# Performance work log

Measured on AMD Instinct MI355X. Metric: run time of the kernel, lower is better.

The kernel has to match this reference:

```python
import jax, jax.numpy as jnp
import numpy as np

NUM_HEADS = 16
DIM = 1024
HID = DIM // NUM_HEADS
B, S = 2, 2048
NEG_INF = -1e30


def setup_inputs() -> dict:
    key = jax.random.key(0)
    ks = jax.random.split(key, 8)
    def xavier(k, shape, fan_in, fan_out):
        limit = np.sqrt(6.0 / (fan_in + fan_out))
        return jax.random.uniform(k, shape, jnp.float32, -limit, limit)
    return {
        "q": jax.random.normal(ks[0], (B, S, DIM), jnp.float32),
        "k": jax.random.normal(ks[1], (B, S, DIM), jnp.float32),
        "v": jax.random.normal(ks[2], (B, S, DIM), jnp.float32),
        "Wq": xavier(ks[3], (1, NUM_HEADS, DIM, HID), DIM, HID),
        "Wk": xavier(ks[4], (1, NUM_HEADS, DIM, HID), DIM, HID),
        "Wv": xavier(ks[5], (1, NUM_HEADS, DIM, HID), DIM, HID),
        "Wo": xavier(ks[6], (1, DIM, DIM), DIM, DIM),
        "mask": jax.random.randint(ks[7], (B, S), 0, 2, jnp.int32),
    }


def reference(q, k, v, Wq, Wk, Wv, Wo, mask):
    b, s, d = q.shape
    norm = jnp.sqrt(jnp.asarray(HID, q.dtype))
    # per-head projections: [B,S,D] x [H,D,hd] -> [B,H,S,hd]
    qh = jnp.einsum('bsd,hde->bhse', q, Wq[0])
    kh = jnp.einsum('bsd,hde->bhse', k, Wk[0])
    vh = jnp.einsum('bsd,hde->bhse', v, Wv[0])
    scores = jnp.einsum('bhse,bhte->bhst', qh, kh) / norm  # [B,H,S,S]
    m = mask.astype(bool)
    # original fills masked rows AND cols with 0.0 (not -inf)
    pad = m[:, None, :, None] | m[:, None, None, :]
    scores = jnp.where(pad, 0.0, scores)
    causal = jnp.triu(jnp.ones((s, s), bool), 1)
    scores = jnp.where(causal, NEG_INF, scores)
    attn = jax.nn.softmax(scores, axis=-1)
    out = jnp.einsum('bhst,bhte->bhse', attn, vh)  # [B,H,S,hd]
    # faithful to original: raw view (memory reinterpretation), NO head transpose
    out = out.reshape(b, s, NUM_HEADS * HID)
    return out @ Wo[0]
```

## Files before the change

kernel.cpp:

```cpp
#include <hip/hip_runtime.h>
#include <hip/hip_bf16.h>

#define BB 2
#define SS 2048
#define DD 1024
#define HH 16
#define HD 64

typedef __attribute__((ext_vector_type(8))) short bf16x8;
typedef __attribute__((ext_vector_type(4))) float floatx4;

__device__ __forceinline__ short f2bf(float x) {
  __hip_bfloat16 h = __float2bfloat16(x);
  return __builtin_bit_cast(short, h);
}

__device__ __forceinline__ unsigned cvtpk_bf16(float lo, float hi) {
  unsigned r;
  asm("v_cvt_pk_bf16_f32 %0, %1, %2" : "=v"(r) : "v"(lo), "v"(hi));
  return r;
}

__device__ __forceinline__ void load_lds16(const void* g, void* l) {
  __builtin_amdgcn_global_load_lds(
      (const __attribute__((address_space(1))) unsigned int*)g,
      (__attribute__((address_space(3))) unsigned int*)l, 16, 0, 0);
}

__device__ __forceinline__ float redsum16(float v) {
  v += __shfl_xor(v, 1, 64);
  v += __shfl_xor(v, 2, 64);
  v += __shfl_xor(v, 4, 64);
  v += __shfl_xor(v, 8, 64);
  return v;
}

__global__ __launch_bounds__(256) void prep(
    const float* __restrict__ q, const float* __restrict__ k,
    const float* __restrict__ v, const float* __restrict__ Wq,
    const float* __restrict__ Wk, const float* __restrict__ Wv,
    const float* __restrict__ Wo, short* __restrict__ qo,
    short* __restrict__ ko, short* __restrict__ vo, short* __restrict__ qT,
    short* __restrict__ kT, short* __restrict__ vT, short* __restrict__ WoT) {
  __shared__ short sT[64 * 72];
  const int blk = blockIdx.x;
  if (blk < 12288) {
    const int which = blk >> 12, x = blk & 4095;
    const float* src = which == 0 ? q : which == 1 ? k : v;
    short* dst       = which == 0 ? qo : which == 1 ? ko : vo;
    size_t i = ((size_t)x * 256 + threadIdx.x) * 4;
    float4 f = *(const float4*)(src + i);
    short4 s;
    s.x = f2bf(f.x); s.y = f2bf(f.y); s.z = f2bf(f.z); s.w = f2bf(f.w);
    *(short4*)(dst + i) = s;
    return;
  }
  const int t = threadIdx.x, r = t >> 2, c0 = (t & 3) * 16;
  const float* src;
  short* dst;
  if (blk < 13056) {
    const int b2 = blk - 12288, which = b2 >> 8, rr = b2 & 255;
    const int dtile = rr & 15, h = rr >> 4, d0 = dtile * 64;
    const float* W = which == 0 ? Wq : which == 1 ? Wk : Wv;
    short* WT      = which == 0 ? qT : which == 1 ? kT : vT;
    src = W + ((size_t)h * DD + d0 + r) * HD + c0;
    dst = WT + ((size_t)h * HD + r) * DD + d0 + c0;
  } else {
    const int b3 = blk - 13056;
    const int k0 = (b3 & 15) * 64, n0 = (b3 >> 4) * 64;
    src = Wo + (size_t)(k0 + r) * DD + n0 + c0;
    dst = WoT + (size_t)(n0 + r) * DD + k0 + c0;
  }
  const float4* s4 = (const float4*)src;
  float4 f0 = s4[0], f1 = s4[1], f2 = s4[2], f3 = s4[3];
  const float ff[16] = {f0.x, f0.y, f0.z, f0.w, f1.x, f1.y, f1.z, f1.w,
                        f2.x, f2.y, f2.z, f2.w, f3.x, f3.y, f3.z, f3.w};
#pragma unroll
  for (int j = 0; j < 16; ++j) sT[r * 72 + c0 + j] = f2bf(ff[j]);
  __syncthreads();
  alignas(16) short tmp[16];
#pragma unroll
  for (int j = 0; j < 16; ++j) tmp[j] = sT[(c0 + j) * 72 + r];
  *(int4*)(dst) = *(const int4*)(tmp);
  *(int4*)(dst + 8) = *(const int4*)(tmp + 8);
}

__global__ __launch_bounds__(256) void proj(
    const short* __restrict__ xq, const short* __restrict__ xk,
    const short* __restrict__ xv, const short* __restrict__ WqT,
    const short* __restrict__ WkT, const short* __restrict__ WvT,
    const int* __restrict__ mask, short* __restrict__ qh,
    short* __restrict__ kh, short* __restrict__ vhT) {
  __shared__ union {
    struct {
      short A[2][128 * 32];
      short B[2][128 * 32];
    } s;
    short tr[64 * 136];
  } u;
  const int xcd = blockIdx.x & 7, tt = blockIdx.x >> 3;
  const int which = tt >> 5;
  const int rest = tt & 31;
  const int j = ((xcd & 3) << 1) | (rest >> 4);
  const int i = ((xcd >> 2) << 4) | (rest & 15);
  const short* X  = which == 0 ? xq : which == 1 ? xk : xv;
  const short* WT = which == 0 ? WqT : which == 1 ? WkT : WvT;
  const int m0 = i * 128, n0 = j * 128;
  const int tid = threadIdx.x, wid = tid >> 6, lane = tid & 63;
  const int quad = lane >> 4, l16 = lane & 15;
  const int wr = wid >> 1, wc = wid & 1;

  auto stage = [&](int buf, int k0) {
#pragma unroll
    for (int ii = 0; ii < 2; ++ii) {
      const int c = wid * 2 + ii;
      const int ci = c * 64 + lane;
      load_lds16(X + (size_t)(m0 + (ci >> 2)) * DD + k0 + (ci & 3) * 8,
                 &u.s.A[buf][c * 512]);
      load_lds16(WT + (size_t)(n0 + (ci >> 2)) * DD + k0 + (ci & 3) * 8,
                 &u.s.B[buf][c * 512]);
    }
  };

  floatx4 acc[4][4] = {};
  stage(0, 0);
  __syncthreads();
  int cur = 0;
  for (int k0 = 0; k0 < DD; k0 += 32) {
    if (k0 + 32 < DD) stage(cur ^ 1, k0 + 32);
    bf16x8 af[4], bfr[4];
#pragma unroll
    for (int mi = 0; mi < 4; ++mi)
      af[mi] =
          *(const bf16x8*)&u.s.A[cur][(wr * 64 + mi * 16 + l16) * 32 +
                                      quad * 8];
#pragma unroll
    for (int ni = 0; ni < 4; ++ni)
      bfr[ni] =
          *(const bf16x8*)&u.s.B[cur][(wc * 64 + ni * 16 + l16) * 32 +
                                      quad * 8];
#pragma unroll
    for (int mi = 0; mi < 4; ++mi)
#pragma unroll
      for (int ni = 0; ni < 4; ++ni)
        acc[mi][ni] = __builtin_amdgcn_mfma_f32_16x16x32_bf16(
            af[mi], bfr[ni], acc[mi][ni], 0, 0, 0);
    __syncthreads();
    cur ^= 1;
  }

  if (which != 2) {
    short* dst = which == 0 ? qh : kh;
    const float scale = (which == 0) ? 0.18033688f : 1.0f;
#pragma unroll
    for (int mi = 0; mi < 4; ++mi)
#pragma unroll
      for (int r2 = 0; r2 < 4; ++r2) {
        const int m = m0 + wr * 64 + mi * 16 + quad * 4 + r2;
        const float rs = mask[m] ? 0.f : scale;
#pragma unroll
        for (int ni = 0; ni < 4; ++ni) {
          const int n = n0 + wc * 64 + ni * 16 + l16;
          dst[(size_t)m * DD + n] = f2bf(acc[mi][ni][r2] * rs);
        }
      }
  } else {
    const int b = m0 >> 11;
#pragma unroll
    for (int p = 0; p < 2; ++p) {
      if (wc == p) {
#pragma unroll
        for (int mi = 0; mi < 4; ++mi)
#pragma unroll
          for (int ni = 0; ni < 4; ++ni)
#pragma unroll
            for (int r2 = 0; r2 < 4; ++r2) {
              const int ml = wr * 64 + mi * 16 + quad * 4 + r2;
              const int nl = ni * 16 + l16;
              u.tr[nl * 136 + ml] = f2bf(acc[mi][ni][r2]);
            }
      }
      __syncthreads();
      const int row = tid >> 2, part = tid & 3;
      const int gn = n0 + p * 64 + row;
      const int h = gn >> 6, e = gn & 63;
      short* dstp = vhT + ((size_t)(b * HH + h) * HD + e) * SS + (m0 & 2047) +
                    part * 32;
      const short* srcl = &u.tr[row * 136 + part * 32];
#pragma unroll
      for (int jj = 0; jj < 4; ++jj)
        *(int4*)(dstp + jj * 8) = *(const int4*)(srcl + jj * 8);
      if (p == 0) __syncthreads();
    }
  }
}

__global__ __launch_bounds__(256, 2) void attn(
    const short* __restrict__ qh, const short* __restrict__ kh,
    const short* __restrict__ vhT, short* __restrict__ X) {
  __shared__ short sm[16384 + 4 * 1152];
  const int tid = threadIdx.x, wid = tid >> 6, lane = tid & 63;
  const int quad = lane >> 4, l16 = lane & 15;
  const int xcd = blockIdx.x & 7, slot = blockIdx.x >> 3;
  const int bh = (xcd << 2) | (slot & 3);
  const int iblk = 31 - (slot >> 2);
  const int nt = iblk + 1;
  const int b = bh >> 4, h = bh & 15;
  const int r0 = iblk * 64;
  const int wrow = r0 + wid * 16;

  const short* Q  = qh + (size_t)b * SS * DD + h * HD;
  const short* K  = kh + (size_t)b * SS * DD + h * HD;
  const short* Vt = vhT + (size_t)bh * HD * SS;
  short* sPw = &sm[16384 + wid * 1152];
  const int swz = (l16 & 7) << 3;

  const int sr0 = tid >> 3, ss0 = (tid & 7) ^ (sr0 & 7);
  const int sr1 = (tid + 256) >> 3, ss1 = (tid & 7) ^ (sr1 & 7);
  const short* pK0 = K + (size_t)sr0 * DD + ss0 * 8;
  const short* pK1 = K + (size_t)sr1 * DD + ss1 * 8;
  const short* pV0 = Vt + (size_t)sr0 * SS + ss0 * 8;
  const short* pV1 = Vt + (size_t)sr1 * SS + ss1 * 8;

  auto stage = [&](int buf, int t) {
    const size_t ko = (size_t)t * 64 * DD;
    const int tc = t * 64;
    short* base = &sm[buf * 8192];
    load_lds16(pK0 + ko, base + tid * 8);
    load_lds16(pK1 + ko, base + 2048 + tid * 8);
    load_lds16(pV0 + tc, base + 4096 + tid * 8);
    load_lds16(pV1 + tc, base + 6144 + tid * 8);
  };

  bf16x8 aq[2];
#pragma unroll
  for (int ks = 0; ks < 2; ++ks)
    aq[ks] = *(const bf16x8*)(Q + (size_t)(wrow + l16) * DD + ks * 32 +
                              quad * 8);

  floatx4 o[4] = {};
  float lacc[4] = {};

  stage(0, 0);
  __syncthreads();
  int cur = 0;
  for (int t = 0; t < nt; ++t) {
    if (t + 1 < nt) stage(cur ^ 1, t + 1);
    const short* kb = &sm[cur * 8192];
    const short* vb = kb + 4096;
    bf16x8 bk[4][2];
#pragma unroll
    for (int ni = 0; ni < 4; ++ni)
#pragma unroll
      for (int ks = 0; ks < 2; ++ks)
        bk[ni][ks] = *(const bf16x8*)&kb[(ni * 16 + l16) * 64 +
                                         ((ks * 32 + quad * 8) ^ swz)];
    floatx4 s[4] = {};
#pragma unroll
    for (int ks = 0; ks < 2; ++ks)
#pragma unroll
      for (int ni = 0; ni < 4; ++ni)
        s[ni] = __builtin_amdgcn_mfma_f32_16x16x32_bf16(aq[ks], bk[ni][ks],
                                                        s[ni], 0, 0, 0);
    const bool diag = (t == nt - 1);
    const int t0 = t * 64;
#pragma unroll
    for (int ni = 0; ni < 4; ++ni)
#pragma unroll
      for (int r2p = 0; r2p < 2; ++r2p) {
        float p0 = __builtin_amdgcn_exp2f(s[ni][2 * r2p]);
        float p1 = __builtin_amdgcn_exp2f(s[ni][2 * r2p + 1]);
        if (diag) {
          const int row = wrow + quad * 4 + 2 * r2p;
          const int col = t0 + ni * 16 + l16;
          if (col > row) p0 = 0.f;
          if (col > row + 1) p1 = 0.f;
        }
        lacc[2 * r2p] += p0;
        lacc[2 * r2p + 1] += p1;
        const unsigned pk = cvtpk_bf16(p0, p1);
        short* wp = &sPw[(quad * 4 + 2 * r2p) * 72 + ni * 16 + l16];
        wp[0] = (short)pk;
        wp[72] = (short)(pk >> 16);
      }
#pragma unroll
    for (int ks = 0; ks < 2; ++ks) {
      const bf16x8 ap =
          *(const bf16x8*)&sPw[l16 * 72 + ks * 32 + quad * 8];
#pragma unroll
      for (int ei = 0; ei < 4; ++ei) {
        const bf16x8 bv = *(const bf16x8*)&vb[(ei * 16 + l16) * 64 +
                                              ((ks * 32 + quad * 8) ^ swz)];
        o[ei] = __builtin_amdgcn_mfma_f32_16x16x32_bf16(ap, bv, o[ei], 0, 0,
                                                        0);
      }
    }
    __syncthreads();
    cur ^= 1;
  }

#pragma unroll
  for (int r2 = 0; r2 < 4; ++r2) {
    const float inv = 1.0f / redsum16(lacc[r2]);
    const int srow = wrow + quad * 4 + r2;
#pragma unroll
    for (int ei = 0; ei < 4; ++ei)
      X[((size_t)bh * SS + srow) * HD + ei * 16 + l16] =
          f2bf(o[ei][r2] * inv);
  }
}

__global__ __launch_bounds__(256) void oproj(const short* __restrict__ X,
                                             const short* __restrict__ WoT,
                                             float* __restrict__ out) {
  __shared__ short sA[2][128 * 32];
  __shared__ short sB[2][64 * 32];
  const int m0 = blockIdx.x * 128, n0 = blockIdx.y * 64;
  const int tid = threadIdx.x, wid = tid >> 6, lane = tid & 63;
  const int quad = lane >> 4, l16 = lane & 15;
  const int wr = wid >> 1, wc = wid & 1;

  auto stage = [&](int buf, int k0) {
#pragma unroll
    for (int i = 0; i < 2; ++i) {
      const int c = wid * 2 + i;
      const int ci = c * 64 + lane;
      load_lds16(X + (size_t)(m0 + (ci >> 2)) * DD + k0 + (ci & 3) * 8,
                 &sA[buf][c * 512]);
    }
    {
      const int ci = wid * 64 + lane;
      load_lds16(WoT + (size_t)(n0 + (ci >> 2)) * DD + k0 + (ci & 3) * 8,
                 &sB[buf][wid * 512]);
    }
  };

  floatx4 acc[4][2] = {};
  stage(0, 0);
  __syncthreads();
  int cur = 0;
  for (int k0 = 0; k0 < DD; k0 += 32) {
    if (k0 + 32 < DD) stage(cur ^ 1, k0 + 32);
    bf16x8 af[4], bfr[2];
#pragma unroll
    for (int mi = 0; mi < 4; ++mi)
      af[mi] = *(const bf16x8*)&sA[cur][(wr * 64 + mi * 16 + l16) * 32 +
                                        quad * 8];
#pragma unroll
    for (int ni = 0; ni < 2; ++ni)
      bfr[ni] = *(const bf16x8*)&sB[cur][(wc * 32 + ni * 16 + l16) * 32 +
                                         quad * 8];
#pragma unroll
    for (int mi = 0; mi < 4; ++mi)
#pragma unroll
      for (int ni = 0; ni < 2; ++ni)
        acc[mi][ni] = __builtin_amdgcn_mfma_f32_16x16x32_bf16(
            af[mi], bfr[ni], acc[mi][ni], 0, 0, 0);
    __syncthreads();
    cur ^= 1;
  }
#pragma unroll
  for (int mi = 0; mi < 4; ++mi)
#pragma unroll
    for (int ni = 0; ni < 2; ++ni)
#pragma unroll
      for (int r2 = 0; r2 < 4; ++r2)
        out[(size_t)(m0 + wr * 64 + mi * 16 + quad * 4 + r2) * DD + n0 +
            wc * 32 + ni * 16 + l16] = acc[mi][ni][r2];
}

extern "C" void kernel_launch(void* const* d_in, const int* in_sizes, int n_in,
                              void* d_out, int out_size, void* d_ws,
                              size_t ws_size, hipStream_t stream) {
  const float* q  = (const float*)d_in[0];
  const float* k  = (const float*)d_in[1];
  const float* v  = (const float*)d_in[2];
  const float* Wq = (const float*)d_in[3];
  const float* Wk = (const float*)d_in[4];
  const float* Wv = (const float*)d_in[5];
  const float* Wo = (const float*)d_in[6];
  const int* mask = (const int*)d_in[7];
  float* out = (float*)d_out;

  short* ws = (short*)d_ws;
  const size_t NIN = (size_t)BB * SS * DD;
  const size_t NWH = (size_t)HH * HD * DD;
  short* qb  = ws;
  short* kb  = ws + NIN;
  short* vb  = ws + 2 * NIN;
  short* WqT = ws + 3 * NIN;
  short* WkT = WqT + NWH;
  short* WvT = WkT + NWH;
  short* WoT = WvT + NWH;
  short* qhp = WoT + (size_t)DD * DD;
  short* khp = qhp + NIN;
  short* vhT = khp + NIN;
  short* Xp  = qb;

  prep<<<dim3(13312), 256, 0, stream>>>(q, k, v, Wq, Wk, Wv, Wo, qb, kb, vb,
                                        WqT, WkT, WvT, WoT);
  proj<<<dim3(768), 256, 0, stream>>>(qb, kb, vb, WqT, WkT, WvT, mask, qhp,
                                      khp, vhT);
  attn<<<dim3(1024), 256, 0, stream>>>(qhp, khp, vhT, Xp);
  oproj<<<dim3(32, 16), 256, 0, stream>>>(Xp, WoT, out);
}
```

Measured before the change: 211.8 us.

## Triple-buffer projection GEMM LDS staging with XOR swizzle and one barrier

Switches the proj and oproj GEMM main loops from double to triple buffering of the LDS tiles. Each iteration now waits on vmcnt for the older prefetch, issues one barrier, and then prefetches two steps ahead. The staged 16-byte chunks are also XOR-swizzled within each row to cut LDS bank conflicts on the fragment reads. The goal is to hide global-load latency and drop one barrier per k-step, at the cost of more LDS, which may lower occupancy, and manual waitcnt counting that has to match the number of loads.

```diff
diff --git a/kernel.cpp b/kernel.cpp
--- a/kernel.cpp
+++ b/kernel.cpp
@@ -93,8 +93,8 @@
     short* __restrict__ kh, short* __restrict__ vhT) {
   __shared__ union {
     struct {
-      short A[2][128 * 32];
-      short B[2][128 * 32];
+      short A[3][128 * 32];
+      short B[3][128 * 32];
     } s;
     short tr[64 * 136];
   } u;
@@ -110,43 +110,49 @@
   const int quad = lane >> 4, l16 = lane & 15;
   const int wr = wid >> 1, wc = wid & 1;
 
-  auto stage = [&](int buf, int k0) {
+  auto stage = [&](int buf, int kk) {
 #pragma unroll
     for (int ii = 0; ii < 2; ++ii) {
       const int c = wid * 2 + ii;
       const int ci = c * 64 + lane;
-      load_lds16(X + (size_t)(m0 + (ci >> 2)) * DD + k0 + (ci & 3) * 8,
+      const int srow = ci >> 2;
+      const int sslot = (ci & 3) ^ ((ci >> 3) & 3);
+      load_lds16(X + (size_t)(m0 + srow) * DD + kk + sslot * 8,
                  &u.s.A[buf][c * 512]);
-      load_lds16(WT + (size_t)(n0 + (ci >> 2)) * DD + k0 + (ci & 3) * 8,
+      load_lds16(WT + (size_t)(n0 + srow) * DD + kk + sslot * 8,
                  &u.s.B[buf][c * 512]);
     }
   };
 
   floatx4 acc[4][4] = {};
+  const int qs = (quad ^ ((l16 >> 1) & 3)) * 8;
   stage(0, 0);
-  __syncthreads();
-  int cur = 0;
+  stage(1, 32);
+  int b0 = 0, b1 = 1, b2 = 2;
   for (int k0 = 0; k0 < DD; k0 += 32) {
-    if (k0 + 32 < DD) stage(cur ^ 1, k0 + 32);
+    if (k0 + 32 < DD)
+      asm volatile("s_waitcnt vmcnt(4)" ::: "memory");
+    else
+      asm volatile("s_waitcnt vmcnt(0)" ::: "memory");
+    __builtin_amdgcn_s_barrier();
+    __builtin_amdgcn_sched_barrier(0);
+    if (k0 + 64 < DD) stage(b2, k0 + 64);
     bf16x8 af[4], bfr[4];
 #pragma unroll
     for (int mi = 0; mi < 4; ++mi)
       af[mi] =
-          *(const bf16x8*)&u.s.A[cur][(wr * 64 + mi * 16 + l16) * 32 +
-                                      quad * 8];
+          *(const bf16x8*)&u.s.A[b0][(wr * 64 + mi * 16 + l16) * 32 + qs];
 #pragma unroll
     for (int ni = 0; ni < 4; ++ni)
       bfr[ni] =
-          *(const bf16x8*)&u.s.B[cur][(wc * 64 + ni * 16 + l16) * 32 +
-                                      quad * 8];
+          *(const bf16x8*)&u.s.B[b0][(wc * 64 + ni * 16 + l16) * 32 + qs];
 #pragma unroll
     for (int mi = 0; mi < 4; ++mi)
 #pragma unroll
       for (int ni = 0; ni < 4; ++ni)
         acc[mi][ni] = __builtin_amdgcn_mfma_f32_16x16x32_bf16(
             af[mi], bfr[ni], acc[mi][ni], 0, 0, 0);
-    __syncthreads();
-    cur ^= 1;
+    const int t = b0; b0 = b1; b1 = b2; b2 = t;
   }
 
   if (which != 2) {
@@ -165,6 +171,7 @@
         }
       }
   } else {
+    __syncthreads();
     const int b = m0 >> 11;
 #pragma unroll
     for (int p = 0; p < 2; ++p) {
@@ -313,51 +320,59 @@
 __global__ __launch_bounds__(256) void oproj(const short* __restrict__ X,
                                              const short* __restrict__ WoT,
                                              float* __restrict__ out) {
-  __shared__ short sA[2][128 * 32];
-  __shared__ short sB[2][64 * 32];
+  __shared__ short sA[3][128 * 32];
+  __shared__ short sB[3][64 * 32];
   const int m0 = blockIdx.x * 128, n0 = blockIdx.y * 64;
   const int tid = threadIdx.x, wid = tid >> 6, lane = tid & 63;
   const int quad = lane >> 4, l16 = lane & 15;
   const int wr = wid >> 1, wc = wid & 1;
 
-  auto stage = [&](int buf, int k0) {
+  auto stage = [&](int buf, int kk) {
 #pragma unroll
     for (int i = 0; i < 2; ++i) {
       const int c = wid * 2 + i;
       const int ci = c * 64 + lane;
-      load_lds16(X + (size_t)(m0 + (ci >> 2)) * DD + k0 + (ci & 3) * 8,
+      const int srow = ci >> 2;
+      const int sslot = (ci & 3) ^ ((ci >> 3) & 3);
+      load_lds16(X + (size_t)(m0 + srow) * DD + kk + sslot * 8,
                  &sA[buf][c * 512]);
     }
     {
       const int ci = wid * 64 + lane;
-      load_lds16(WoT + (size_t)(n0 + (ci >> 2)) * DD + k0 + (ci & 3) * 8,
+      const int srow = ci >> 2;
+      const int sslot = (ci & 3) ^ ((ci >> 3) & 3);
+      load_lds16(WoT + (size_t)(n0 + srow) * DD + kk + sslot * 8,
                  &sB[buf][wid * 512]);
     }
   };
 
   floatx4 acc[4][2] = {};
+  const int qs = (quad ^ ((l16 >> 1) & 3)) * 8;
   stage(0, 0);
-  __syncthreads();
-  int cur = 0;
+  stage(1, 32);
+  int b0 = 0, b1 = 1, b2 = 2;
   for (int k0 = 0; k0 < DD; k0 += 32) {
-    if (k0 + 32 < DD) stage(cur ^ 1, k0 + 32);
+    if (k0 + 32 < DD)
+      asm volatile("s_waitcnt vmcnt(3)" ::: "memory");
+    else
+      asm volatile("s_waitcnt vmcnt(0)" ::: "memory");
+    __builtin_amdgcn_s_barrier();
+    __builtin_amdgcn_sched_barrier(0);
+    if (k0 + 64 < DD) stage(b2, k0 + 64);
     bf16x8 af[4], bfr[2];
 #pragma unroll
     for (int mi = 0; mi < 4; ++mi)
-      af[mi] = *(const bf16x8*)&sA[cur][(wr * 64 + mi * 16 + l16) * 32 +
-                                        quad * 8];
+      af[mi] = *(const bf16x8*)&sA[b0][(wr * 64 + mi * 16 + l16) * 32 + qs];
 #pragma unroll
     for (int ni = 0; ni < 2; ++ni)
-      bfr[ni] = *(const bf16x8*)&sB[cur][(wc * 32 + ni * 16 + l16) * 32 +
-                                         quad * 8];
+      bfr[ni] = *(const bf16x8*)&sB[b0][(wc * 32 + ni * 16 + l16) * 32 + qs];
 #pragma unroll
     for (int mi = 0; mi < 4; ++mi)
 #pragma unroll
       for (int ni = 0; ni < 2; ++ni)
         acc[mi][ni] = __builtin_amdgcn_mfma_f32_16x16x32_bf16(
             af[mi], bfr[ni], acc[mi][ni], 0, 0, 0);
-    __syncthreads();
-    cur ^= 1;
+    const int t = b0; b0 = b1; b1 = b2; b2 = t;
   }
 #pragma unroll
   for (int mi = 0; mi < 4; ++mi)
```

After: 203.3 us. 4.0% less time.
